# Kernel optimization log

Hardware: AMD Instinct MI355X
Metric: run time of the kernel (lower is better)

Reference implementation:

```python
import jax, jax.numpy as jnp
import numpy as np

B, S, H = 4, 2048, 1024
NH, HD = 16, 64
P = 64            # num persistent vectors
INTER = 2048      # memory MLP intermediate size
LR, MOM, WD = 0.01, 0.9, 0.01
EPS = 1e-12


def setup_inputs() -> dict:
    key = jax.random.key(0)
    ks = jax.random.split(key, 12)
    inp = {
        'hidden_states': jax.random.normal(ks[0], (B, S, H), jnp.float32),
        'k_mem': jax.random.normal(ks[1], (B, S, H), jnp.float32),
        'v_mem': jax.random.normal(ks[2], (B, S, H), jnp.float32),
        # persistent-memory params
        'persistent_vectors': jax.random.normal(ks[3], (P, H), jnp.float32) * 0.02,
        'Wq': jax.random.normal(ks[4], (H, H), jnp.float32) * 0.02,
        'bq': jnp.zeros((H,), jnp.float32),
        'Wo': jax.random.normal(ks[5], (H, H), jnp.float32) * 0.02,
        'bo': jnp.zeros((H,), jnp.float32),
        'ln_g': jnp.ones((H,), jnp.float32),
        'ln_b': jnp.zeros((H,), jnp.float32),
        # surprise-memory MLP params (x @ W1 + b1 -> relu -> @ W2 + b2)
        'W1': jax.random.normal(ks[6], (H, INTER), jnp.float32) * 0.02,
        'b1': jnp.zeros((INTER,), jnp.float32),
        'W2': jax.random.normal(ks[7], (INTER, H), jnp.float32) * 0.02,
        'b2': jnp.zeros((H,), jnp.float32),
        # momentum buffers
        'mW1': jnp.zeros((H, INTER), jnp.float32),
        'mb1': jnp.zeros((INTER,), jnp.float32),
        'mW2': jnp.zeros((INTER, H), jnp.float32),
        'mb2': jnp.zeros((H,), jnp.float32),
    }
    return inp


def _layernorm(x, g, b):
    mu = jnp.mean(x, axis=-1, keepdims=True)
    var = jnp.var(x, axis=-1, keepdims=True)
    return (x - mu) * jax.lax.rsqrt(var + EPS) * g + b


def _mlp(x, W1, b1, W2, b2):
    return jax.nn.relu(x @ W1 + b1) @ W2 + b2


def reference(hidden_states, k_mem, v_mem, persistent_vectors, Wq, bq, Wo, bo,
              ln_g, ln_b, W1, b1, W2, b2, mW1, mb1, mW2, mb2):
    # ---- PersistentMemory: cross-attention to persistent vectors ----
    residual = hidden_states
    hs_norm = _layernorm(hidden_states, ln_g, ln_b)
    q = hs_norm @ Wq + bq                                   # [B,S,H]
    q = q.reshape(B, S, NH, HD).transpose(0, 2, 1, 3)        # [B,nh,S,hd]
    kv = persistent_vectors.reshape(P, NH, HD).transpose(1, 0, 2)  # [nh,P,hd]
    scores = jnp.einsum('bhsd,hpd->bhsp', q, kv) / jnp.sqrt(jnp.float32(HD))
    probs = jax.nn.softmax(scores, axis=-1)
    attn = jnp.einsum('bhsp,hpd->bhsd', probs, kv)           # [B,nh,S,hd]
    attn = attn.transpose(0, 2, 1, 3).reshape(B, S, H)
    out1 = residual + (attn @ Wo + bo)

    # ---- SurpriseMemoryMLP: test-time SGD-with-momentum update (no outer grad) ----
    k_flat = jax.lax.stop_gradient(k_mem.reshape(-1, H))
    v_flat = jax.lax.stop_gradient(v_mem.reshape(-1, H))

    def assoc_loss(params):
        w1, bb1, w2, bb2 = params
        pred = _mlp(k_flat, w1, bb1, w2, bb2)
        return jnp.mean((pred - v_flat) ** 2)

    params = (jax.lax.stop_gradient(W1), jax.lax.stop_gradient(b1),
              jax.lax.stop_gradient(W2), jax.lax.stop_gradient(b2))
    loss, grads = jax.value_and_grad(assoc_loss)(params)

    def upd(p, m, g):
        new_m = MOM * m - LR * g
        return (1.0 - WD) * p + new_m, new_m
    nW1, _ = upd(params[0], mW1, grads[0])
    nb1, _ = upd(params[1], mb1, grads[1])
    nW2, _ = upd(params[2], mW2, grads[2])
    nb2, _ = upd(params[3], mb2, grads[3])

    # ---- query updated memory (torch.no_grad -> stop_gradient) ----
    mem_out = _mlp(out1.reshape(-1, H), nW1, nb1, nW2, nb2).reshape(B, S, H)
    mem_out = jax.lax.stop_gradient(mem_out)

    return out1 + mem_out
```

## Files before the change

### kernel.cpp

```cpp
#include <hip/hip_runtime.h>
#include <hip/hip_bf16.h>

constexpr int B  = 4;
constexpr int S  = 2048;
constexpr int H  = 1024;
constexpr int NH = 16;
constexpr int HD = 64;
constexpr int P  = 64;
constexpr int INTER = 2048;
constexpr int M  = B * S;

typedef __bf16  bf16x8  __attribute__((ext_vector_type(8)));
typedef float   floatx4 __attribute__((ext_vector_type(4)));

#define AS1 __attribute__((address_space(1)))
#define AS3 __attribute__((address_space(3)))

__global__ __launch_bounds__(256) void mc_ln_kernel(
    const float* __restrict__ x, const float* __restrict__ g,
    const float* __restrict__ b, __bf16* __restrict__ y)
{
    int row = blockIdx.x;
    const float4* xr = (const float4*)(x + (size_t)row * H);
    float4 v = xr[threadIdx.x];
    float s  = v.x + v.y + v.z + v.w;
    float s2 = v.x*v.x + v.y*v.y + v.z*v.z + v.w*v.w;
    #pragma unroll
    for (int off = 32; off > 0; off >>= 1) {
        s  += __shfl_down(s,  off);
        s2 += __shfl_down(s2, off);
    }
    __shared__ float ws1[4], ws2[4];
    __shared__ float smu, srv;
    int lane = threadIdx.x & 63, wid = threadIdx.x >> 6;
    if (lane == 0) { ws1[wid] = s; ws2[wid] = s2; }
    __syncthreads();
    if (threadIdx.x == 0) {
        float t1 = ws1[0] + ws1[1] + ws1[2] + ws1[3];
        float t2 = ws2[0] + ws2[1] + ws2[2] + ws2[3];
        float mu  = t1 * (1.0f / H);
        float var = t2 * (1.0f / H) - mu * mu;
        smu = mu;
        srv = rsqrtf(var + 1e-12f);
    }
    __syncthreads();
    float mu = smu, rv = srv;
    float4 gv = ((const float4*)g)[threadIdx.x];
    float4 bv = ((const float4*)b)[threadIdx.x];
    union { ushort4 u; __bf16 h[4]; } pk;
    pk.h[0] = (__bf16)((v.x - mu) * rv * gv.x + bv.x);
    pk.h[1] = (__bf16)((v.y - mu) * rv * gv.y + bv.y);
    pk.h[2] = (__bf16)((v.z - mu) * rv * gv.z + bv.z);
    pk.h[3] = (__bf16)((v.w - mu) * rv * gv.w + bv.w);
    ((ushort4*)(y + (size_t)row * H))[threadIdx.x] = pk.u;
}

__global__ __launch_bounds__(256) void mc_trans_kernel(
    const float* __restrict__ src0, const float* __restrict__ mom0,
    __bf16* __restrict__ dst0,
    const float* __restrict__ src1, const float* __restrict__ mom1,
    __bf16* __restrict__ dst1,
    int Rdim, int Cdim, int do_upd)
{
    const float* src = blockIdx.z ? src1 : src0;
    const float* mom = blockIdx.z ? mom1 : mom0;
    __bf16*      dst = blockIdx.z ? dst1 : dst0;
    __shared__ float ts[32][33];
    int c0 = blockIdx.x * 32, r0 = blockIdx.y * 32;
    int tx = threadIdx.x & 31, ty0 = threadIdx.x >> 5;
    #pragma unroll
    for (int i = 0; i < 4; i++) {
        int r = ty0 + i * 8;
        size_t idx = (size_t)(r0 + r) * Cdim + c0 + tx;
        float v = src[idx];
        if (do_upd) v = 0.99f * v + 0.9f * mom[idx];
        ts[r][tx] = v;
    }
    __syncthreads();
    #pragma unroll
    for (int i = 0; i < 4; i++) {
        int r = ty0 + i * 8;
        dst[(size_t)(c0 + r) * Rdim + r0 + tx] = (__bf16)ts[tx][r];
    }
}

__global__ void mc_upd_kernel(const float* __restrict__ b1, const float* __restrict__ mb1,
                              float* __restrict__ nb1,
                              const float* __restrict__ b2, const float* __restrict__ mb2,
                              float* __restrict__ nb2)
{
    int i = blockIdx.x * blockDim.x + threadIdx.x;
    if (i < INTER) nb1[i] = 0.99f * b1[i] + 0.9f * mb1[i];
    else {
        int j = i - INTER;
        if (j < H) nb2[j] = 0.99f * b2[j] + 0.9f * mb2[j];
    }
}

__global__ __launch_bounds__(256) void mc_gemm_bt(
    const __bf16* __restrict__ A, const __bf16* __restrict__ Bt,
    const float* __restrict__ bias, const float* __restrict__ res,
    float* __restrict__ outF, __bf16* __restrict__ outB,
    int Ndim, int Kdim, int do_relu)
{
    __shared__ __bf16 As[128 * 32];
    __shared__ __bf16 Bs[128 * 32];

    int tid  = threadIdx.x;
    int lane = tid & 63;
    int w    = tid >> 6;
    int wm   = (w >> 1) * 64;
    int wn   = (w & 1) * 64;
    int l16  = lane & 15;
    int quad = lane >> 4;

    int m0 = blockIdx.y * 128, n0 = blockIdx.x * 128;

    floatx4 acc[4][4] = {};

    for (int k0 = 0; k0 < Kdim; k0 += 32) {
        #pragma unroll
        for (int t = 0; t < 2; t++) {
            int f = t * 256 + tid;
            int r = f >> 2, c8 = (f & 3) * 8;
            __builtin_amdgcn_global_load_lds(
                (const AS1 void*)(A + (size_t)(m0 + r) * Kdim + k0 + c8),
                (AS3 void*)(As + f * 8), 16, 0, 0);
        }
        #pragma unroll
        for (int t = 0; t < 2; t++) {
            int f = t * 256 + tid;
            int r = f >> 2, c8 = (f & 3) * 8;
            __builtin_amdgcn_global_load_lds(
                (const AS1 void*)(Bt + (size_t)(n0 + r) * Kdim + k0 + c8),
                (AS3 void*)(Bs + f * 8), 16, 0, 0);
        }
        __syncthreads();

        bf16x8 af[4], bfr[4];
        #pragma unroll
        for (int i = 0; i < 4; i++)
            af[i] = *(const bf16x8*)&As[(wm + i * 16 + l16) * 32 + quad * 8];
        #pragma unroll
        for (int j = 0; j < 4; j++)
            bfr[j] = *(const bf16x8*)&Bs[(wn + j * 16 + l16) * 32 + quad * 8];
        #pragma unroll
        for (int i = 0; i < 4; i++)
            #pragma unroll
            for (int j = 0; j < 4; j++)
                acc[i][j] = __builtin_amdgcn_mfma_f32_16x16x32_bf16(
                    af[i], bfr[j], acc[i][j], 0, 0, 0);
        __syncthreads();
    }

    #pragma unroll
    for (int i = 0; i < 4; i++) {
        #pragma unroll
        for (int j = 0; j < 4; j++) {
            int col = n0 + wn + j * 16 + l16;
            float bv = bias ? bias[col] : 0.0f;
            #pragma unroll
            for (int r = 0; r < 4; r++) {
                int row = m0 + wm + i * 16 + quad * 4 + r;
                size_t idx = (size_t)row * Ndim + col;
                float v = acc[i][j][r] + bv;
                if (res)     v += res[idx];
                if (do_relu) v  = fmaxf(v, 0.0f);
                if (outF) outF[idx] = v;
                if (outB) outB[idx] = (__bf16)v;
            }
        }
    }
}

constexpr int ATT_LD = 72;

__global__ __launch_bounds__(256) void mc_attn_mfma(
    const __bf16* __restrict__ q, const float* __restrict__ pv,
    __bf16* __restrict__ attn)
{
    __shared__ __bf16 Qs[128 * ATT_LD];
    __shared__ __bf16 Ks[64 * ATT_LD];
    __shared__ __bf16 KTs[64 * ATT_LD];
    __shared__ __bf16 Ps[128 * ATT_LD];

    int blk = blockIdx.x;
    int st  = blk & 15;
    int bh  = blk >> 4;
    int b   = bh >> 4;
    int h   = bh & 15;
    int s0  = st * 128;
    size_t qbase = ((size_t)(b * S + s0)) * H + h * HD;

    int tid  = threadIdx.x;
    int lane = tid & 63;
    int w    = tid >> 6;
    int l16  = lane & 15;
    int quad = lane >> 4;

    #pragma unroll
    for (int it = 0; it < 4; it++) {
        int c = it * 256 + tid;
        int row = c >> 3, cc = c & 7;
        float4 v = *(const float4*)(q + qbase + (size_t)row * H + cc * 8);
        *(float4*)&Qs[row * ATT_LD + cc * 8] = v;
    }
    for (int i = tid; i < 64 * 64; i += 256) {
        int p = i >> 6, d = i & 63;
        __bf16 bv = (__bf16)pv[(size_t)p * H + h * HD + d];
        Ks[p * ATT_LD + d]  = bv;
        KTs[d * ATT_LD + p] = bv;
    }
    __syncthreads();

    int rbase = w * 32;
    floatx4 sc[2][4] = {};
    #pragma unroll
    for (int ks = 0; ks < 2; ks++) {
        bf16x8 aq[2], bk[4];
        #pragma unroll
        for (int i = 0; i < 2; i++)
            aq[i] = *(const bf16x8*)&Qs[(rbase + i * 16 + l16) * ATT_LD + ks * 32 + quad * 8];
        #pragma unroll
        for (int j = 0; j < 4; j++)
            bk[j] = *(const bf16x8*)&Ks[(j * 16 + l16) * ATT_LD + ks * 32 + quad * 8];
        #pragma unroll
        for (int i = 0; i < 2; i++)
            #pragma unroll
            for (int j = 0; j < 4; j++)
                sc[i][j] = __builtin_amdgcn_mfma_f32_16x16x32_bf16(aq[i], bk[j], sc[i][j], 0, 0, 0);
    }

    #pragma unroll
    for (int i = 0; i < 2; i++) {
        #pragma unroll
        for (int r = 0; r < 4; r++) {
            float v0 = sc[i][0][r] * 0.125f;
            float v1 = sc[i][1][r] * 0.125f;
            float v2 = sc[i][2][r] * 0.125f;
            float v3 = sc[i][3][r] * 0.125f;
            float mx = fmaxf(fmaxf(v0, v1), fmaxf(v2, v3));
            #pragma unroll
            for (int off = 8; off > 0; off >>= 1) mx = fmaxf(mx, __shfl_xor(mx, off));
            float e0 = __expf(v0 - mx), e1 = __expf(v1 - mx);
            float e2 = __expf(v2 - mx), e3 = __expf(v3 - mx);
            float sm = e0 + e1 + e2 + e3;
            #pragma unroll
            for (int off = 8; off > 0; off >>= 1) sm += __shfl_xor(sm, off);
            float inv = __frcp_rn(sm);
            int row = rbase + i * 16 + quad * 4 + r;
            Ps[row * ATT_LD +  0 + l16] = (__bf16)(e0 * inv);
            Ps[row * ATT_LD + 16 + l16] = (__bf16)(e1 * inv);
            Ps[row * ATT_LD + 32 + l16] = (__bf16)(e2 * inv);
            Ps[row * ATT_LD + 48 + l16] = (__bf16)(e3 * inv);
        }
    }
    __syncthreads();

    floatx4 ov[2][4] = {};
    #pragma unroll
    for (int ks = 0; ks < 2; ks++) {
        bf16x8 ap[2], bkt[4];
        #pragma unroll
        for (int i = 0; i < 2; i++)
            ap[i] = *(const bf16x8*)&Ps[(rbase + i * 16 + l16) * ATT_LD + ks * 32 + quad * 8];
        #pragma unroll
        for (int j = 0; j < 4; j++)
            bkt[j] = *(const bf16x8*)&KTs[(j * 16 + l16) * ATT_LD + ks * 32 + quad * 8];
        #pragma unroll
        for (int i = 0; i < 2; i++)
            #pragma unroll
            for (int j = 0; j < 4; j++)
                ov[i][j] = __builtin_amdgcn_mfma_f32_16x16x32_bf16(ap[i], bkt[j], ov[i][j], 0, 0, 0);
    }

    #pragma unroll
    for (int i = 0; i < 2; i++) {
        #pragma unroll
        for (int j = 0; j < 4; j++) {
            int col = j * 16 + l16;
            #pragma unroll
            for (int r = 0; r < 4; r++) {
                int row = rbase + i * 16 + quad * 4 + r;
                attn[qbase + (size_t)row * H + col] = (__bf16)ov[i][j][r];
            }
        }
    }
}

extern "C" void kernel_launch(void* const* d_in, const int* in_sizes, int n_in,
                              void* d_out, int out_size, void* d_ws, size_t ws_size,
                              hipStream_t stream)
{
    const float* hidden = (const float*)d_in[0];
    const float* pv   = (const float*)d_in[3];
    const float* Wq   = (const float*)d_in[4];
    const float* bq   = (const float*)d_in[5];
    const float* Wo   = (const float*)d_in[6];
    const float* bo   = (const float*)d_in[7];
    const float* ln_g = (const float*)d_in[8];
    const float* ln_b = (const float*)d_in[9];
    const float* W1   = (const float*)d_in[10];
    const float* b1   = (const float*)d_in[11];
    const float* W2   = (const float*)d_in[12];
    const float* b2   = (const float*)d_in[13];
    const float* mW1  = (const float*)d_in[14];
    const float* mb1  = (const float*)d_in[15];
    const float* mW2  = (const float*)d_in[16];
    const float* mb2  = (const float*)d_in[17];

    float* out = (float*)d_out;
    char*  wsb = (char*)d_ws;

    constexpr size_t MB = 1024 * 1024;
    __bf16* qb     = (__bf16*)(wsb);
    __bf16* normb  = (__bf16*)(wsb + 16  * MB);
    __bf16* attnb  = (__bf16*)(wsb + 32  * MB);
    __bf16* out1b  = (__bf16*)(wsb + 48  * MB);
    __bf16* hb     = (__bf16*)(wsb + 64  * MB);
    __bf16* Wqt    = (__bf16*)(wsb + 96  * MB);
    __bf16* Wot    = (__bf16*)(wsb + 98  * MB);
    __bf16* W1t    = (__bf16*)(wsb + 100 * MB);
    __bf16* W2t    = (__bf16*)(wsb + 104 * MB);
    float*  nb1    = (float*) (wsb + 108 * MB);
    float*  nb2    = (float*) (wsb + 108 * MB + 8192);

    mc_trans_kernel<<<dim3(32, 32, 2), 256, 0, stream>>>(
        Wq, nullptr, Wqt, Wo, nullptr, Wot, H, H, 0);
    mc_trans_kernel<<<dim3(64, 32, 1), 256, 0, stream>>>(
        W1, mW1, W1t, nullptr, nullptr, nullptr, H, INTER, 1);
    mc_trans_kernel<<<dim3(32, 64, 1), 256, 0, stream>>>(
        W2, mW2, W2t, nullptr, nullptr, nullptr, INTER, H, 1);
    mc_upd_kernel<<<(INTER + H + 255) / 256, 256, 0, stream>>>(b1, mb1, nb1, b2, mb2, nb2);

    mc_ln_kernel<<<M, 256, 0, stream>>>(hidden, ln_g, ln_b, normb);

    dim3 gH(H / 128, M / 128);
    mc_gemm_bt<<<gH, 256, 0, stream>>>(normb, Wqt, bq, nullptr, nullptr, qb, H, H, 0);

    mc_attn_mfma<<<B * NH * (S / 128), 256, 0, stream>>>(qb, pv, attnb);

    mc_gemm_bt<<<gH, 256, 0, stream>>>(attnb, Wot, bo, hidden, out, out1b, H, H, 0);

    dim3 gI(INTER / 128, M / 128);
    mc_gemm_bt<<<gI, 256, 0, stream>>>(out1b, W1t, nb1, nullptr, nullptr, hb, INTER, H, 1);

    mc_gemm_bt<<<gH, 256, 0, stream>>>(hb, W2t, nb2, out, out, nullptr, H, INTER, 0);
}
```

Baseline: 425.2 us.

## Double GEMM K-tile to 64 with XOR-swizzled LDS and bf16 residual reuse

```diff
diff --git a/kernel.cpp b/kernel.cpp
--- a/kernel.cpp
+++ b/kernel.cpp
@@ -99,12 +99,13 @@
 
 __global__ __launch_bounds__(256) void mc_gemm_bt(
     const __bf16* __restrict__ A, const __bf16* __restrict__ Bt,
-    const float* __restrict__ bias, const float* __restrict__ res,
+    const float* __restrict__ bias,
+    const float* __restrict__ resF, const __bf16* __restrict__ resB,
     float* __restrict__ outF, __bf16* __restrict__ outB,
     int Ndim, int Kdim, int do_relu)
 {
-    __shared__ __bf16 As[128 * 32];
-    __shared__ __bf16 Bs[128 * 32];
+    __shared__ __bf16 As[128 * 64];
+    __shared__ __bf16 Bs[128 * 64];
 
     int tid  = threadIdx.x;
     int lane = tid & 63;
@@ -113,43 +114,48 @@
     int wn   = (w & 1) * 64;
     int l16  = lane & 15;
     int quad = lane >> 4;
+    int sw   = l16 & 7;
 
     int m0 = blockIdx.y * 128, n0 = blockIdx.x * 128;
 
     floatx4 acc[4][4] = {};
 
-    for (int k0 = 0; k0 < Kdim; k0 += 32) {
-        #pragma unroll
-        for (int t = 0; t < 2; t++) {
+    for (int k0 = 0; k0 < Kdim; k0 += 64) {
+        #pragma unroll
+        for (int t = 0; t < 4; t++) {
             int f = t * 256 + tid;
-            int r = f >> 2, c8 = (f & 3) * 8;
+            int r = f >> 3, c = (f & 7) ^ (r & 7);
             __builtin_amdgcn_global_load_lds(
-                (const AS1 void*)(A + (size_t)(m0 + r) * Kdim + k0 + c8),
+                (const AS1 void*)(A + (size_t)(m0 + r) * Kdim + k0 + c * 8),
                 (AS3 void*)(As + f * 8), 16, 0, 0);
         }
         #pragma unroll
-        for (int t = 0; t < 2; t++) {
+        for (int t = 0; t < 4; t++) {
             int f = t * 256 + tid;
-            int r = f >> 2, c8 = (f & 3) * 8;
+            int r = f >> 3, c = (f & 7) ^ (r & 7);
             __builtin_amdgcn_global_load_lds(
-                (const AS1 void*)(Bt + (size_t)(n0 + r) * Kdim + k0 + c8),
+                (const AS1 void*)(Bt + (size_t)(n0 + r) * Kdim + k0 + c * 8),
                 (AS3 void*)(Bs + f * 8), 16, 0, 0);
         }
         __syncthreads();
 
-        bf16x8 af[4], bfr[4];
-        #pragma unroll
-        for (int i = 0; i < 4; i++)
-            af[i] = *(const bf16x8*)&As[(wm + i * 16 + l16) * 32 + quad * 8];
-        #pragma unroll
-        for (int j = 0; j < 4; j++)
-            bfr[j] = *(const bf16x8*)&Bs[(wn + j * 16 + l16) * 32 + quad * 8];
-        #pragma unroll
-        for (int i = 0; i < 4; i++)
+        #pragma unroll
+        for (int ks = 0; ks < 2; ks++) {
+            int cq = ((ks << 2) | quad) ^ sw;
+            bf16x8 af[4], bfr[4];
+            #pragma unroll
+            for (int i = 0; i < 4; i++)
+                af[i] = *(const bf16x8*)&As[(wm + i * 16 + l16) * 64 + cq * 8];
             #pragma unroll
             for (int j = 0; j < 4; j++)
-                acc[i][j] = __builtin_amdgcn_mfma_f32_16x16x32_bf16(
-                    af[i], bfr[j], acc[i][j], 0, 0, 0);
+                bfr[j] = *(const bf16x8*)&Bs[(wn + j * 16 + l16) * 64 + cq * 8];
+            #pragma unroll
+            for (int i = 0; i < 4; i++)
+                #pragma unroll
+                for (int j = 0; j < 4; j++)
+                    acc[i][j] = __builtin_amdgcn_mfma_f32_16x16x32_bf16(
+                        af[i], bfr[j], acc[i][j], 0, 0, 0);
+        }
         __syncthreads();
     }
 
@@ -164,7 +170,8 @@
                 int row = m0 + wm + i * 16 + quad * 4 + r;
                 size_t idx = (size_t)row * Ndim + col;
                 float v = acc[i][j][r] + bv;
-                if (res)     v += res[idx];
+                if (resF)    v += resF[idx];
+                if (resB)    v += (float)resB[idx];
                 if (do_relu) v  = fmaxf(v, 0.0f);
                 if (outF) outF[idx] = v;
                 if (outB) outB[idx] = (__bf16)v;
@@ -336,14 +343,18 @@
     mc_ln_kernel<<<M, 256, 0, stream>>>(hidden, ln_g, ln_b, normb);
 
     dim3 gH(H / 128, M / 128);
-    mc_gemm_bt<<<gH, 256, 0, stream>>>(normb, Wqt, bq, nullptr, nullptr, qb, H, H, 0);
+    mc_gemm_bt<<<gH, 256, 0, stream>>>(normb, Wqt, bq, nullptr, nullptr,
+                                       nullptr, qb, H, H, 0);
 
     mc_attn_mfma<<<B * NH * (S / 128), 256, 0, stream>>>(qb, pv, attnb);
 
-    mc_gemm_bt<<<gH, 256, 0, stream>>>(attnb, Wot, bo, hidden, out, out1b, H, H, 0);
+    mc_gemm_bt<<<gH, 256, 0, stream>>>(attnb, Wot, bo, hidden, nullptr,
+                                       nullptr, out1b, H, H, 0);
 
     dim3 gI(INTER / 128, M / 128);
-    mc_gemm_bt<<<gI, 256, 0, stream>>>(out1b, W1t, nb1, nullptr, nullptr, hb, INTER, H, 1);
-
-    mc_gemm_bt<<<gH, 256, 0, stream>>>(hb, W2t, nb2, out, out, nullptr, H, INTER, 0);
-}
+    mc_gemm_bt<<<gI, 256, 0, stream>>>(out1b, W1t, nb1, nullptr, nullptr,
+                                       nullptr, hb, INTER, H, 1);
+
+    mc_gemm_bt<<<gH, 256, 0, stream>>>(hb, W2t, nb2, nullptr, out1b,
+                                       out, nullptr, H, INTER, 0);
+}
```

New measurement: 386.2 us. 9.2% less time.
